# Kernel optimization log

Hardware: AMD Instinct MI355X
Metric: run time of the kernel (lower is better)

The kernel has to match this reference:

```python
import jax, jax.numpy as jnp
import numpy as np

C_Z = 128
C_HIDDEN = 32
N_HEAD = 4
HC = N_HEAD * C_HIDDEN  # 128
LN_EPS = 1e-5


def setup_inputs() -> dict:
    key = jax.random.key(0)
    ks = jax.random.split(key, 8)
    b, n = 1, 256
    s = 1.0 / np.sqrt(C_Z)
    return {
        "z_ij": jax.random.normal(ks[0], (b, n, n, C_Z), dtype=jnp.float32),
        "ln_gamma": jnp.ones((C_Z,), dtype=jnp.float32),
        "ln_beta": jnp.zeros((C_Z,), dtype=jnp.float32),
        "Wq": jax.random.normal(ks[1], (C_Z, HC), dtype=jnp.float32) * s,
        "Wk": jax.random.normal(ks[2], (C_Z, HC), dtype=jnp.float32) * s,
        "Wv": jax.random.normal(ks[3], (C_Z, HC), dtype=jnp.float32) * s,
        "Wb": jax.random.normal(ks[4], (C_Z, N_HEAD), dtype=jnp.float32) * s,
        "Wg": jax.random.normal(ks[5], (C_Z, HC), dtype=jnp.float32) * s,
        "Wout": jax.random.normal(ks[6], (HC, C_Z), dtype=jnp.float32) * (1.0 / np.sqrt(HC)),
    }


def reference(z_ij, ln_gamma, ln_beta, Wq, Wk, Wv, Wb, Wg, Wout):
    b, n, _, _ = z_ij.shape
    # LayerNorm over c_z
    mu = jnp.mean(z_ij, axis=-1, keepdims=True)
    var = jnp.var(z_ij, axis=-1, keepdims=True)
    z = (z_ij - mu) * jax.lax.rsqrt(var + LN_EPS) * ln_gamma + ln_beta

    def heads(x):  # [b,i,j,hc] -> [b,i,j,h,d]
        return x.reshape(b, n, n, N_HEAD, C_HIDDEN)

    q = heads(z @ Wq)
    k = heads(z @ Wk)
    v = heads(z @ Wv)
    bias = z @ Wb                      # [b,i,j,h]
    g = jax.nn.sigmoid(heads(z @ Wg))  # [b,i,j,h,d]

    scores = jnp.einsum('bijhd,bikhd->bijkh', q, k) / np.sqrt(C_HIDDEN)
    scores = scores + bias[:, None]    # bias[b, j, k, h] broadcast over i
    a = jax.nn.softmax(scores, axis=-2)  # over k
    o = jnp.einsum('bijkh,bikhd->bijhd', a, v)
    o = (g * o).reshape(b, n, n, HC)
    return o @ Wout
```

## Files before the change

kernel.cpp:

```cpp
#include <hip/hip_runtime.h>

typedef _Float16 f16x8 __attribute__((ext_vector_type(8)));
typedef _Float16 f16x2 __attribute__((ext_vector_type(2)));
typedef float f32x4 __attribute__((ext_vector_type(4)));

#define MFMA16(a, b, c) __builtin_amdgcn_mfma_f32_16x16x32_f16(a, b, c, 0, 0, 0)

#define NROW 65536
#define SEGB 16777216ull

__global__ __launch_bounds__(256) void k_ln(
    const float* __restrict__ z, const float* __restrict__ gamma,
    const float* __restrict__ beta, const float* __restrict__ Wb,
    const float* __restrict__ Wq, const float* __restrict__ Wk,
    const float* __restrict__ Wv, const float* __restrict__ Wg,
    const float* __restrict__ Wout,
    _Float16* __restrict__ zln, float* __restrict__ biasT,
    _Float16* __restrict__ WtAll)
{
  __shared__ _Float16 sw[32 * 136];
  int bid = blockIdx.x;
  if (bid < 16384) {
    int lane = threadIdx.x & 63;
    int w = threadIdx.x >> 6;
    int row = bid * 4 + w;
    float2 v = ((const float2*)(z + (size_t)row * 128))[lane];
    float s = v.x + v.y;
    #pragma unroll
    for (int m = 1; m < 64; m <<= 1) s += __shfl_xor(s, m);
    float mu = s * 0.0078125f;
    float dx = v.x - mu, dy = v.y - mu;
    float q = dx * dx + dy * dy;
    #pragma unroll
    for (int m = 1; m < 64; m <<= 1) q += __shfl_xor(q, m);
    float rs = rsqrtf(q * 0.0078125f + 1e-5f);
    float2 g2 = ((const float2*)gamma)[lane];
    float2 b2 = ((const float2*)beta)[lane];
    float y0 = dx * rs * g2.x + b2.x;
    float y1 = dy * rs * g2.y + b2.y;
    f16x2 pr; pr.x = (_Float16)y0; pr.y = (_Float16)y1;
    *(f16x2*)(zln + (size_t)row * 128 + 2 * lane) = pr;
    float4 wb0 = ((const float4*)Wb)[2 * lane];
    float4 wb1 = ((const float4*)Wb)[2 * lane + 1];
    float pb0 = y0 * wb0.x + y1 * wb1.x;
    float pb1 = y0 * wb0.y + y1 * wb1.y;
    float pb2 = y0 * wb0.z + y1 * wb1.z;
    float pb3 = y0 * wb0.w + y1 * wb1.w;
    #pragma unroll
    for (int m = 1; m < 64; m <<= 1) {
      pb0 += __shfl_xor(pb0, m);
      pb1 += __shfl_xor(pb1, m);
      pb2 += __shfl_xor(pb2, m);
      pb3 += __shfl_xor(pb3, m);
    }
    if (lane == 0) {
      biasT[row] = pb0;
      biasT[NROW + row] = pb1;
      biasT[2 * NROW + row] = pb2;
      biasT[3 * NROW + row] = pb3;
    }
  } else {
    int t = bid - 16384;
    int mat = t >> 2, n0 = (t & 3) * 32;
    const float* src = (mat == 0) ? Wq : (mat == 1) ? Wk : (mat == 2) ? Wv
                       : (mat == 3) ? Wg : Wout;
    _Float16* dst = WtAll + mat * 16384;
    for (int it = 0; it < 16; ++it) {
      int e = threadIdx.x + it * 256;
      int c = e >> 5, j = e & 31;
      sw[j * 136 + c] = (_Float16)src[c * 128 + n0 + j];
    }
    __syncthreads();
    for (int it = 0; it < 2; ++it) {
      int ch = threadIdx.x + it * 256;
      int n = ch >> 4, k8 = (ch & 15) * 8;
      *(int4*)(dst + (n0 + n) * 128 + k8) = *(const int4*)&sw[n * 136 + k8];
    }
  }
}

__global__ __launch_bounds__(256) void k_proj(
    const _Float16* __restrict__ A, const _Float16* __restrict__ WtAll,
    _Float16* __restrict__ Qb, _Float16* __restrict__ Kb,
    _Float16* __restrict__ Vb, _Float16* __restrict__ Gb)
{
  __shared__ _Float16 sA[128 * 136];
  __shared__ _Float16 sB[128 * 136];
  int m0 = blockIdx.x * 128;
  int by = blockIdx.y;
  const _Float16* Bt = WtAll + by * 16384;
  _Float16* outp = (by == 0) ? Qb : (by == 1) ? Kb : (by == 2) ? Vb : Gb;
  int tid = threadIdx.x;
  for (int it = 0; it < 8; ++it) {
    int ch = tid + it * 256;
    int r = ch >> 4, c8 = (ch & 15) * 8;
    *(int4*)&sA[r * 136 + c8] = *(const int4*)(A + (size_t)(m0 + r) * 128 + c8);
    *(int4*)&sB[r * 136 + c8] = *(const int4*)(Bt + r * 128 + c8);
  }
  __syncthreads();
  int lane = tid & 63, w = tid >> 6;
  int mw = (w >> 1) * 64, nw = (w & 1) * 64;
  int lr = lane & 15, lg = lane >> 4;
  f32x4 z4 = {0.f, 0.f, 0.f, 0.f};
  f32x4 acc[4][4];
  #pragma unroll
  for (int mt = 0; mt < 4; ++mt)
    #pragma unroll
    for (int nt = 0; nt < 4; ++nt) acc[mt][nt] = z4;
  #pragma unroll
  for (int k0 = 0; k0 < 128; k0 += 32) {
    f16x8 af[4], bf[4];
    #pragma unroll
    for (int mt = 0; mt < 4; ++mt)
      af[mt] = *(const f16x8*)&sA[(mw + mt * 16 + lr) * 136 + k0 + lg * 8];
    #pragma unroll
    for (int nt = 0; nt < 4; ++nt)
      bf[nt] = *(const f16x8*)&sB[(nw + nt * 16 + lr) * 136 + k0 + lg * 8];
    #pragma unroll
    for (int mt = 0; mt < 4; ++mt)
      #pragma unroll
      for (int nt = 0; nt < 4; ++nt)
        acc[mt][nt] = MFMA16(af[mt], bf[nt], acc[mt][nt]);
  }
  bool sig = (by == 3);
  #pragma unroll
  for (int mt = 0; mt < 4; ++mt)
    #pragma unroll
    for (int nt = 0; nt < 4; ++nt)
      #pragma unroll
      for (int r = 0; r < 4; ++r) {
        int row = m0 + mw + mt * 16 + lg * 4 + r;
        int col = nw + nt * 16 + lr;
        float v = acc[mt][nt][r];
        if (sig) v = 1.0f / (1.0f + __expf(-v));
        outp[(size_t)row * 128 + col] = (_Float16)v;
      }
}

__global__ __launch_bounds__(256) void k_attn(
    const _Float16* __restrict__ Qb, const _Float16* __restrict__ Kb,
    const _Float16* __restrict__ Vb, const _Float16* __restrict__ Gb,
    const float* __restrict__ biasT, _Float16* __restrict__ OG)
{
  __shared__ _Float16 sK[256 * 32];
  __shared__ _Float16 sV[32 * 256];
  __shared__ _Float16 sP[64 * 256];
  int i = blockIdx.x, h = blockIdx.y;
  int tid = threadIdx.x;
  size_t base = ((size_t)i * 256) * 128 + h * 32;
  for (int it = 0; it < 4; ++it) {
    int ch = tid + it * 256;
    int r = ch >> 2, cx = ch & 3;
    int p = cx ^ ((r >> 1) & 3);
    *(int4*)&sK[r * 32 + p * 8] = *(const int4*)(Kb + base + (size_t)r * 128 + cx * 8);
  }
  for (int it = 0; it < 4; ++it) {
    int ch = tid + it * 256;
    int k = ch >> 2, d8 = (ch & 3) * 8;
    f16x8 tv = *(const f16x8*)(Vb + base + (size_t)k * 128 + d8);
    #pragma unroll
    for (int jj = 0; jj < 8; ++jj) {
      int d = d8 + jj;
      int p = (k >> 3) ^ (d & 7);
      sV[d * 256 + p * 8 + (k & 7)] = tv[jj];
    }
  }
  __syncthreads();
  int lane = tid & 63, w = tid >> 6;
  int lr = lane & 15, lg = lane >> 4;
  const float scale = 0.17677669529663687f;
  f32x4 z4 = {0.f, 0.f, 0.f, 0.f};
  for (int pass = 0; pass < 4; ++pass) {
    int jbase = pass * 64;
    int jq = jbase + w * 16 + lr;
    f16x8 aq = *(const f16x8*)(Qb + base + (size_t)jq * 128 + lg * 8);
    f32x4 sacc[16];
    #pragma unroll
    for (int kt = 0; kt < 16; ++kt) {
      int r = kt * 16 + lr;
      int p = lg ^ ((r >> 1) & 3);
      f16x8 bk = *(const f16x8*)&sK[r * 32 + p * 8];
      sacc[kt] = MFMA16(aq, bk, z4);
    }
    #pragma unroll
    for (int r = 0; r < 4; ++r) {
      int j = jbase + w * 16 + lg * 4 + r;
      const float* brow = biasT + (size_t)h * NROW + (size_t)j * 256;
      float mx = -1e30f;
      #pragma unroll
      for (int kt = 0; kt < 16; ++kt) {
        float sv = sacc[kt][r] * scale + brow[kt * 16 + lr];
        sacc[kt][r] = sv;
        mx = fmaxf(mx, sv);
      }
      #pragma unroll
      for (int msk = 1; msk < 16; msk <<= 1) mx = fmaxf(mx, __shfl_xor(mx, msk));
      float sum = 0.f;
      #pragma unroll
      for (int kt = 0; kt < 16; ++kt) {
        float pv = __expf(sacc[kt][r] - mx);
        sacc[kt][r] = pv;
        sum += pv;
      }
      #pragma unroll
      for (int msk = 1; msk < 16; msk <<= 1) sum += __shfl_xor(sum, msk);
      float rinv = 1.0f / sum;
      int row = w * 16 + lg * 4 + r;
      #pragma unroll
      for (int kt = 0; kt < 16; ++kt) {
        int k = kt * 16 + lr;
        int pch = (k >> 3) ^ (row & 7);
        sP[row * 256 + pch * 8 + (k & 7)] = (_Float16)(sacc[kt][r] * rinv);
      }
    }
    f32x4 oacc[2] = {z4, z4};
    int prow = w * 16 + lr;
    #pragma unroll
    for (int ks = 0; ks < 8; ++ks) {
      int c = ks * 4 + lg;
      f16x8 ap = *(const f16x8*)&sP[prow * 256 + (c ^ (prow & 7)) * 8];
      #pragma unroll
      for (int nt = 0; nt < 2; ++nt) {
        int d = nt * 16 + lr;
        f16x8 bv = *(const f16x8*)&sV[d * 256 + (c ^ (d & 7)) * 8];
        oacc[nt] = MFMA16(ap, bv, oacc[nt]);
      }
    }
    #pragma unroll
    for (int nt = 0; nt < 2; ++nt)
      #pragma unroll
      for (int r = 0; r < 4; ++r) {
        int j = jbase + w * 16 + lg * 4 + r;
        int d = nt * 16 + lr;
        size_t idx = base + (size_t)j * 128 + d;
        float g = (float)Gb[idx];
        OG[idx] = (_Float16)(oacc[nt][r] * g);
      }
  }
}

__global__ __launch_bounds__(256) void k_outp(
    const _Float16* __restrict__ A, const _Float16* __restrict__ Bt,
    float* __restrict__ out)
{
  __shared__ _Float16 sA[128 * 136];
  __shared__ _Float16 sB[128 * 136];
  int m0 = blockIdx.x * 128;
  int tid = threadIdx.x;
  for (int it = 0; it < 8; ++it) {
    int ch = tid + it * 256;
    int r = ch >> 4, c8 = (ch & 15) * 8;
    *(int4*)&sA[r * 136 + c8] = *(const int4*)(A + (size_t)(m0 + r) * 128 + c8);
    *(int4*)&sB[r * 136 + c8] = *(const int4*)(Bt + r * 128 + c8);
  }
  __syncthreads();
  int lane = tid & 63, w = tid >> 6;
  int mw = (w >> 1) * 64, nw = (w & 1) * 64;
  int lr = lane & 15, lg = lane >> 4;
  f32x4 z4 = {0.f, 0.f, 0.f, 0.f};
  f32x4 acc[4][4];
  #pragma unroll
  for (int mt = 0; mt < 4; ++mt)
    #pragma unroll
    for (int nt = 0; nt < 4; ++nt) acc[mt][nt] = z4;
  #pragma unroll
  for (int k0 = 0; k0 < 128; k0 += 32) {
    f16x8 af[4], bf[4];
    #pragma unroll
    for (int mt = 0; mt < 4; ++mt)
      af[mt] = *(const f16x8*)&sA[(mw + mt * 16 + lr) * 136 + k0 + lg * 8];
    #pragma unroll
    for (int nt = 0; nt < 4; ++nt)
      bf[nt] = *(const f16x8*)&sB[(nw + nt * 16 + lr) * 136 + k0 + lg * 8];
    #pragma unroll
    for (int mt = 0; mt < 4; ++mt)
      #pragma unroll
      for (int nt = 0; nt < 4; ++nt)
        acc[mt][nt] = MFMA16(af[mt], bf[nt], acc[mt][nt]);
  }
  #pragma unroll
  for (int mt = 0; mt < 4; ++mt)
    #pragma unroll
    for (int nt = 0; nt < 4; ++nt)
      #pragma unroll
      for (int r = 0; r < 4; ++r) {
        int row = m0 + mw + mt * 16 + lg * 4 + r;
        int col = nw + nt * 16 + lr;
        out[(size_t)row * 128 + col] = acc[mt][nt][r];
      }
}

extern "C" void kernel_launch(void* const* d_in, const int* in_sizes, int n_in,
                              void* d_out, int out_size, void* d_ws, size_t ws_size,
                              hipStream_t stream) {
  (void)in_sizes; (void)n_in; (void)out_size; (void)ws_size;
  const float* z    = (const float*)d_in[0];
  const float* gam  = (const float*)d_in[1];
  const float* bet  = (const float*)d_in[2];
  const float* Wq   = (const float*)d_in[3];
  const float* Wk   = (const float*)d_in[4];
  const float* Wv   = (const float*)d_in[5];
  const float* Wb   = (const float*)d_in[6];
  const float* Wg   = (const float*)d_in[7];
  const float* Wout = (const float*)d_in[8];

  char* ws = (char*)d_ws;
  _Float16* zln   = (_Float16*)(ws);
  _Float16* Qb    = (_Float16*)(ws + SEGB);
  _Float16* Kb    = (_Float16*)(ws + SEGB * 2);
  _Float16* Vb    = (_Float16*)(ws + SEGB * 3);
  _Float16* Gb    = (_Float16*)(ws + SEGB * 4);
  float*    biasT = (float*)   (ws + SEGB * 5);
  _Float16* WtAll = (_Float16*)(ws + SEGB * 5 + 1048576);

  k_ln<<<16404, 256, 0, stream>>>(z, gam, bet, Wb, Wq, Wk, Wv, Wg, Wout,
                                  zln, biasT, WtAll);
  k_proj<<<dim3(512, 4), 256, 0, stream>>>(zln, WtAll, Qb, Kb, Vb, Gb);
  k_attn<<<dim3(256, 4), 256, 0, stream>>>(Qb, Kb, Vb, Gb, biasT, zln);
  k_outp<<<512, 256, 0, stream>>>(zln, WtAll + 4 * 16384, (float*)d_out);
}
```

Baseline: 203.1 us.

## Keep softmax probabilities in registers and transpose bias for coalesced loads

The attention kernel now computes the score tile transposed (K as the A operand), so each lane holds a column of scores. Max and sum reduce with only two shuffles, and exp2 runs with log2e folded into the scale and the bias. The shared-memory P buffer is removed: probabilities are packed to fp16 and redistributed with lane shuffles into the MFMA A-operand layout, and normalisation is deferred to the output. The bias table is stored transposed so loads coalesce. Also adds MFMA priority hints, an occupancy bound of 4 blocks, and a remapped projection grid that groups the four weight matrices per row block for L2 reuse. The trade-off is many more cross-lane shuffles, plus occupancy-limited register pressure.

```diff
diff --git a/kernel.cpp b/kernel.cpp
--- a/kernel.cpp
+++ b/kernel.cpp
@@ -3,11 +3,13 @@
 typedef _Float16 f16x8 __attribute__((ext_vector_type(8)));
 typedef _Float16 f16x2 __attribute__((ext_vector_type(2)));
 typedef float f32x4 __attribute__((ext_vector_type(4)));
+typedef int i32x4 __attribute__((ext_vector_type(4)));
 
 #define MFMA16(a, b, c) __builtin_amdgcn_mfma_f32_16x16x32_f16(a, b, c, 0, 0, 0)
 
 #define NROW 65536
 #define SEGB 16777216ull
+#define LOG2E 1.4426950408889634f
 
 __global__ __launch_bounds__(256) void k_ln(
     const float* __restrict__ z, const float* __restrict__ gamma,
@@ -54,10 +56,11 @@
       pb3 += __shfl_xor(pb3, m);
     }
     if (lane == 0) {
-      biasT[row] = pb0;
-      biasT[NROW + row] = pb1;
-      biasT[2 * NROW + row] = pb2;
-      biasT[3 * NROW + row] = pb3;
+      int tix = ((row & 255) << 8) + (row >> 8);
+      biasT[tix] = pb0 * LOG2E;
+      biasT[NROW + tix] = pb1 * LOG2E;
+      biasT[2 * NROW + tix] = pb2 * LOG2E;
+      biasT[3 * NROW + tix] = pb3 * LOG2E;
     }
   } else {
     int t = bid - 16384;
@@ -86,8 +89,10 @@
 {
   __shared__ _Float16 sA[128 * 136];
   __shared__ _Float16 sB[128 * 136];
-  int m0 = blockIdx.x * 128;
-  int by = blockIdx.y;
+  int e = blockIdx.x;
+  int by = (e >> 3) & 3;
+  int xb = ((e >> 5) << 3) | (e & 7);
+  int m0 = xb * 128;
   const _Float16* Bt = WtAll + by * 16384;
   _Float16* outp = (by == 0) ? Qb : (by == 1) ? Kb : (by == 2) ? Vb : Gb;
   int tid = threadIdx.x;
@@ -137,14 +142,13 @@
       }
 }
 
-__global__ __launch_bounds__(256) void k_attn(
+__global__ __launch_bounds__(256, 4) void k_attn(
     const _Float16* __restrict__ Qb, const _Float16* __restrict__ Kb,
     const _Float16* __restrict__ Vb, const _Float16* __restrict__ Gb,
     const float* __restrict__ biasT, _Float16* __restrict__ OG)
 {
   __shared__ _Float16 sK[256 * 32];
   __shared__ _Float16 sV[32 * 256];
-  __shared__ _Float16 sP[64 * 256];
   int i = blockIdx.x, h = blockIdx.y;
   int tid = threadIdx.x;
   size_t base = ((size_t)i * 256) * 128 + h * 32;
@@ -168,73 +172,99 @@
   __syncthreads();
   int lane = tid & 63, w = tid >> 6;
   int lr = lane & 15, lg = lane >> 4;
-  const float scale = 0.17677669529663687f;
+  const float scale = 0.2550348858f;
   f32x4 z4 = {0.f, 0.f, 0.f, 0.f};
+  int la = lr + ((lg & 1) << 5);
+  int lb = la + 16;
+  int hi = lg >> 1;
   for (int pass = 0; pass < 4; ++pass) {
     int jbase = pass * 64;
-    int jq = jbase + w * 16 + lr;
-    f16x8 aq = *(const f16x8*)(Qb + base + (size_t)jq * 128 + lg * 8);
+    int jg = jbase + (w << 4) + lr;
+    f16x8 aq = *(const f16x8*)(Qb + base + (size_t)jg * 128 + lg * 8);
     f32x4 sacc[16];
+    __builtin_amdgcn_s_setprio(1);
     #pragma unroll
     for (int kt = 0; kt < 16; ++kt) {
       int r = kt * 16 + lr;
       int p = lg ^ ((r >> 1) & 3);
       f16x8 bk = *(const f16x8*)&sK[r * 32 + p * 8];
-      sacc[kt] = MFMA16(aq, bk, z4);
-    }
-    #pragma unroll
-    for (int r = 0; r < 4; ++r) {
-      int j = jbase + w * 16 + lg * 4 + r;
-      const float* brow = biasT + (size_t)h * NROW + (size_t)j * 256;
-      float mx = -1e30f;
-      #pragma unroll
-      for (int kt = 0; kt < 16; ++kt) {
-        float sv = sacc[kt][r] * scale + brow[kt * 16 + lr];
-        sacc[kt][r] = sv;
-        mx = fmaxf(mx, sv);
-      }
-      #pragma unroll
-      for (int msk = 1; msk < 16; msk <<= 1) mx = fmaxf(mx, __shfl_xor(mx, msk));
-      float sum = 0.f;
-      #pragma unroll
-      for (int kt = 0; kt < 16; ++kt) {
-        float pv = __expf(sacc[kt][r] - mx);
-        sacc[kt][r] = pv;
-        sum += pv;
-      }
-      #pragma unroll
-      for (int msk = 1; msk < 16; msk <<= 1) sum += __shfl_xor(sum, msk);
-      float rinv = 1.0f / sum;
-      int row = w * 16 + lg * 4 + r;
-      #pragma unroll
-      for (int kt = 0; kt < 16; ++kt) {
-        int k = kt * 16 + lr;
-        int pch = (k >> 3) ^ (row & 7);
-        sP[row * 256 + pch * 8 + (k & 7)] = (_Float16)(sacc[kt][r] * rinv);
-      }
-    }
+      sacc[kt] = MFMA16(bk, aq, z4);
+    }
+    __builtin_amdgcn_s_setprio(0);
+    const float* bp = biasT + ((size_t)h << 16) + ((lg * 4) << 8) + jg;
+    float mx = -1e30f;
+    #pragma unroll
+    for (int kt = 0; kt < 16; ++kt) {
+      const float* bb = bp + (kt << 12);
+      float b0 = bb[0], b1 = bb[256], b2 = bb[512], b3 = bb[768];
+      sacc[kt][0] = sacc[kt][0] * scale + b0;
+      sacc[kt][1] = sacc[kt][1] * scale + b1;
+      sacc[kt][2] = sacc[kt][2] * scale + b2;
+      sacc[kt][3] = sacc[kt][3] * scale + b3;
+      mx = fmaxf(mx, fmaxf(fmaxf(sacc[kt][0], sacc[kt][1]),
+                           fmaxf(sacc[kt][2], sacc[kt][3])));
+    }
+    mx = fmaxf(mx, __shfl_xor(mx, 16));
+    mx = fmaxf(mx, __shfl_xor(mx, 32));
+    float sum = 0.f;
+    int q16[16][2];
+    #pragma unroll
+    for (int kt = 0; kt < 16; ++kt) {
+      float p0 = exp2f(sacc[kt][0] - mx);
+      float p1 = exp2f(sacc[kt][1] - mx);
+      float p2 = exp2f(sacc[kt][2] - mx);
+      float p3 = exp2f(sacc[kt][3] - mx);
+      sum += (p0 + p1) + (p2 + p3);
+      f16x2 w01, w23;
+      w01.x = (_Float16)p0; w01.y = (_Float16)p1;
+      w23.x = (_Float16)p2; w23.y = (_Float16)p3;
+      q16[kt][0] = __builtin_bit_cast(int, w01);
+      q16[kt][1] = __builtin_bit_cast(int, w23);
+    }
+    sum += __shfl_xor(sum, 16);
+    sum += __shfl_xor(sum, 32);
+    float rinv = 1.0f / sum;
+    float rr0 = __shfl(rinv, (lg << 2));
+    float rr1 = __shfl(rinv, (lg << 2) + 1);
+    float rr2 = __shfl(rinv, (lg << 2) + 2);
+    float rr3 = __shfl(rinv, (lg << 2) + 3);
     f32x4 oacc[2] = {z4, z4};
-    int prow = w * 16 + lr;
     #pragma unroll
     for (int ks = 0; ks < 8; ++ks) {
-      int c = ks * 4 + lg;
-      f16x8 ap = *(const f16x8*)&sP[prow * 256 + (c ^ (prow & 7)) * 8];
+      int a0 = __shfl(q16[2 * ks][0], la);
+      int a1 = __shfl(q16[2 * ks][1], la);
+      int c0 = __shfl(q16[2 * ks + 1][0], la);
+      int c1 = __shfl(q16[2 * ks + 1][1], la);
+      int b0 = __shfl(q16[2 * ks][0], lb);
+      int b1 = __shfl(q16[2 * ks][1], lb);
+      int d0 = __shfl(q16[2 * ks + 1][0], lb);
+      int d1 = __shfl(q16[2 * ks + 1][1], lb);
+      i32x4 wv;
+      wv.x = hi ? c0 : a0;
+      wv.y = hi ? c1 : a1;
+      wv.z = hi ? d0 : b0;
+      wv.w = hi ? d1 : b1;
+      f16x8 ap = __builtin_bit_cast(f16x8, wv);
+      __builtin_amdgcn_s_setprio(1);
       #pragma unroll
       for (int nt = 0; nt < 2; ++nt) {
         int d = nt * 16 + lr;
+        int c = ks * 4 + lg;
         f16x8 bv = *(const f16x8*)&sV[d * 256 + (c ^ (d & 7)) * 8];
         oacc[nt] = MFMA16(ap, bv, oacc[nt]);
       }
-    }
+      __builtin_amdgcn_s_setprio(0);
+    }
+    float rrs[4] = {rr0, rr1, rr2, rr3};
     #pragma unroll
     for (int nt = 0; nt < 2; ++nt)
       #pragma unroll
       for (int r = 0; r < 4; ++r) {
-        int j = jbase + w * 16 + lg * 4 + r;
+        int j = jbase + (w << 4) + (lg << 2) + r;
         int d = nt * 16 + lr;
         size_t idx = base + (size_t)j * 128 + d;
         float g = (float)Gb[idx];
-        OG[idx] = (_Float16)(oacc[nt][r] * g);
+        OG[idx] = (_Float16)(oacc[nt][r] * rrs[r] * g);
       }
   }
 }
@@ -315,7 +345,7 @@
 
   k_ln<<<16404, 256, 0, stream>>>(z, gam, bet, Wb, Wq, Wk, Wv, Wg, Wout,
                                   zln, biasT, WtAll);
-  k_proj<<<dim3(512, 4), 256, 0, stream>>>(zln, WtAll, Qb, Kb, Vb, Gb);
+  k_proj<<<2048, 256, 0, stream>>>(zln, WtAll, Qb, Kb, Vb, Gb);
   k_attn<<<dim3(256, 4), 256, 0, stream>>>(Qb, Kb, Vb, Gb, biasT, zln);
   k_outp<<<512, 256, 0, stream>>>(zln, WtAll + 4 * 16384, (float*)d_out);
 }
```

Result: slower. 253.7 us (+24.9%).
